# Kernel optimization log

Measured on AMD Instinct MI355X. Metric: run time of the kernel, lower is better.

Reference implementation:

```python
import jax, jax.numpy as jnp
import numpy as np

N_NODES = 100000
N_EDGES = 1600000
D_IN = 128
D_OUT = 128

def setup_inputs() -> dict:
    key = jax.random.key(0)
    k1, k2, k3, k4, k5 = jax.random.split(key, 5)
    h = jax.random.normal(k1, (N_NODES, D_IN), dtype=jnp.float32)
    src = jax.random.randint(k2, (N_EDGES,), 0, N_NODES, dtype=jnp.int64)
    dst = jax.random.randint(k3, (N_EDGES,), 0, N_NODES, dtype=jnp.int64)
    # Xavier-ish init for the two linear maps (fc_self, fc_neigh), no bias
    scale = 1.0 / np.sqrt(D_IN)
    W_self = jax.random.normal(k4, (D_IN, D_OUT), dtype=jnp.float32) * scale
    W_neigh = jax.random.normal(k5, (D_IN, D_OUT), dtype=jnp.float32) * scale
    return {"h": h, "src": src, "dst": dst, "W_self": W_self, "W_neigh": W_neigh}

def reference(h, src, dst, W_self, W_neigh):
    # DGL SAGEConv mean aggregator, bias=False:
    #   h_neigh[v] = mean_{(u->v) in E} h[u]   (0 if v has no in-edges)
    #   out = h @ W_self + h_neigh @ W_neigh
    msg = h[src]  # [E, D_IN] neighbor gather
    neigh_sum = jax.ops.segment_sum(msg, dst, num_segments=N_NODES)  # [N, D_IN]
    deg = jax.ops.segment_sum(jnp.ones((src.shape[0],), dtype=h.dtype), dst,
                              num_segments=N_NODES)  # [N]
    h_neigh = neigh_sum / jnp.maximum(deg, 1.0)[:, None]
    return h @ W_self + h_neigh @ W_neigh
```

## Files before the change

### kernel.cpp

```cpp
#include <hip/hip_runtime.h>


constexpr int NN = 100000;
constexpr int NE = 1600000;
constexpr int D  = 128;
constexpr int BK = 64;
constexpr int NB = (NN + BK - 1) / BK;
constexpr int PB = 8192;
constexpr int CAPB = 2048;
constexpr int XSTN = 136;
constexpr int PADI = 32;
constexpr int CVT_BLOCKS = NN * D / 8 / 256;

typedef __attribute__((ext_vector_type(8))) short short8;
typedef __attribute__((ext_vector_type(4))) float floatx4;
typedef __attribute__((ext_vector_type(2))) float floatx2;

static __device__ __forceinline__ unsigned short f2bf(float f) {
    unsigned u = __float_as_uint(f);
    unsigned r = ((u >> 16) & 1u) + 0x7fffu;
    return (unsigned short)((u + r) >> 16);
}

__global__ __launch_bounds__(256) void k_cvt(
    const float* __restrict__ h, const float* __restrict__ Wself,
    const float* __restrict__ Wneigh, uint2* __restrict__ hf8,
    unsigned short* __restrict__ Wp)
{
    const int t = threadIdx.x;
    if (blockIdx.x < CVT_BLOCKS) {
        int i = blockIdx.x * 256 + t;
        const float4* h4 = (const float4*)h;
        float4 a = h4[(size_t)i * 2];
        float4 b = h4[(size_t)i * 2 + 1];
        unsigned q0 = __builtin_amdgcn_cvt_pk_fp8_f32(a.x, a.y, 0u, false);
        q0          = __builtin_amdgcn_cvt_pk_fp8_f32(a.z, a.w, q0, true);
        unsigned q1 = __builtin_amdgcn_cvt_pk_fp8_f32(b.x, b.y, 0u, false);
        q1          = __builtin_amdgcn_cvt_pk_fp8_f32(b.z, b.w, q1, true);
        hf8[i] = make_uint2(q0, q1);
    } else {
        int kg  = (blockIdx.x - CVT_BLOCKS) * 2 + (t >> 7);
        int col = t & 127;
        unsigned short v[8];
#pragma unroll
        for (int j = 0; j < 8; ++j) {
            int k = kg * 8 + j;
            const float* W = (k < 128) ? (Wself + (size_t)k * D)
                                       : (Wneigh + (size_t)(k - 128) * D);
            v[j] = f2bf(W[col]);
        }
        uint4 o;
        o.x = (unsigned)v[0] | ((unsigned)v[1] << 16);
        o.y = (unsigned)v[2] | ((unsigned)v[3] << 16);
        o.z = (unsigned)v[4] | ((unsigned)v[5] << 16);
        o.w = (unsigned)v[6] | ((unsigned)v[7] << 16);
        ((uint4*)Wp)[kg * 128 + col] = o;
    }
}

__global__ __launch_bounds__(256) void k_part(
    const int* __restrict__ src, const int* __restrict__ dst,
    int* __restrict__ bcursor, unsigned* __restrict__ packed)
{
    __shared__ int lh[NB];
    const int t = threadIdx.x;
    const int e0 = blockIdx.x * PB;

    for (int i = t; i < NB; i += 256) lh[i] = 0;
    __syncthreads();

    int myd[32], msrc[32];
#pragma unroll
    for (int j = 0; j < 32; ++j) {
        int e = e0 + j * 256 + t;
        myd[j] = (e < NE) ? dst[e] : -1;
    }
#pragma unroll
    for (int j = 0; j < 32; ++j) {
        int e = e0 + j * 256 + t;
        msrc[j] = (e < NE) ? src[e] : 0;
    }
#pragma unroll
    for (int j = 0; j < 32; ++j)
        if (myd[j] >= 0) atomicAdd(&lh[myd[j] >> 6], 1);
    __syncthreads();
    for (int i = t; i < NB; i += 256) {
        int c = lh[i];
        if (c) lh[i] = atomicAdd(&bcursor[(size_t)i * PADI], c);
    }
    __syncthreads();
#pragma unroll
    for (int j = 0; j < 32; ++j) {
        if (myd[j] >= 0) {
            int b = myd[j] >> 6;
            int pos = atomicAdd(&lh[b], 1);
            packed[(size_t)b * CAPB + pos] =
                (unsigned)msrc[j] | ((unsigned)(myd[j] & 63) << 17);
        }
    }
}

__global__ __launch_bounds__(512, 8) void k_agg_gemm(
    const float* __restrict__ h, const uint2* __restrict__ hf8,
    const int* __restrict__ bcursor, const unsigned* __restrict__ packed,
    const unsigned short* __restrict__ Wp, float* __restrict__ out)
{
    __shared__ unsigned short Xs[BK][XSTN];
    __shared__ unsigned sorted[CAPB];
    __shared__ int cnt[BK], offs[BK], cur[BK];

    const int t      = threadIdx.x;
    const int bucket = blockIdx.x;
    const size_t ebeg = (size_t)bucket * CAPB;
    const int ecnt   = min(bcursor[(size_t)bucket * PADI], CAPB);

    if (t < BK) cnt[t] = 0;
    __syncthreads();

    unsigned pk[4];
#pragma unroll
    for (int i = 0; i < 4; ++i) {
        int idx = t + i * 512;
        pk[i] = (idx < ecnt) ? packed[ebeg + idx] : 0u;
    }
#pragma unroll
    for (int i = 0; i < 4; ++i) {
        int idx = t + i * 512;
        if (idx < ecnt) atomicAdd(&cnt[(pk[i] >> 17) & 63u], 1);
    }
    __syncthreads();
    if (t < BK) {
        int v = cnt[t];
        int sum = v;
#pragma unroll
        for (int off = 1; off < 64; off <<= 1) {
            int u = __shfl_up(sum, off, 64);
            if (t >= off) sum += u;
        }
        offs[t] = sum - v;
        cur[t]  = sum - v;
    }
    __syncthreads();
#pragma unroll
    for (int i = 0; i < 4; ++i) {
        int idx = t + i * 512;
        if (idx < ecnt) {
            int pos = atomicAdd(&cur[(pk[i] >> 17) & 63u], 1);
            sorted[pos] = pk[i] & 0x1FFFFu;
        }
    }
    __syncthreads();

    const int slot = t >> 4;
    const int l16  = t & 15;
#pragma unroll
    for (int ni = 0; ni < 2; ++ni) {
        int node = slot + ni * 32;
        const int beg = offs[node];
        const int n   = cnt[node];
        float a0[8] = {0,0,0,0,0,0,0,0};
        float a1[8] = {0,0,0,0,0,0,0,0};
        float a2[8] = {0,0,0,0,0,0,0,0};
        float a3[8] = {0,0,0,0,0,0,0,0};
        int e = 0;
        for (; e + 7 < n; e += 8) {
            uint2 x0 = hf8[(size_t)sorted[beg + e]     * 16 + l16];
            uint2 x1 = hf8[(size_t)sorted[beg + e + 1] * 16 + l16];
            uint2 x2 = hf8[(size_t)sorted[beg + e + 2] * 16 + l16];
            uint2 x3 = hf8[(size_t)sorted[beg + e + 3] * 16 + l16];
            uint2 x4 = hf8[(size_t)sorted[beg + e + 4] * 16 + l16];
            uint2 x5 = hf8[(size_t)sorted[beg + e + 5] * 16 + l16];
            uint2 x6 = hf8[(size_t)sorted[beg + e + 6] * 16 + l16];
            uint2 x7 = hf8[(size_t)sorted[beg + e + 7] * 16 + l16];
#pragma unroll
            for (int half = 0; half < 2; ++half) {
                unsigned w0 = half ? x0.y : x0.x, w1 = half ? x1.y : x1.x;
                unsigned w2 = half ? x2.y : x2.x, w3 = half ? x3.y : x3.x;
                unsigned w4 = half ? x4.y : x4.x, w5 = half ? x5.y : x5.x;
                unsigned w6 = half ? x6.y : x6.x, w7 = half ? x7.y : x7.x;
                floatx2 p;
                p = __builtin_amdgcn_cvt_pk_f32_fp8(w0, false); a0[half*4+0]+=p.x; a0[half*4+1]+=p.y;
                p = __builtin_amdgcn_cvt_pk_f32_fp8(w0, true);  a0[half*4+2]+=p.x; a0[half*4+3]+=p.y;
                p = __builtin_amdgcn_cvt_pk_f32_fp8(w1, false); a1[half*4+0]+=p.x; a1[half*4+1]+=p.y;
                p = __builtin_amdgcn_cvt_pk_f32_fp8(w1, true);  a1[half*4+2]+=p.x; a1[half*4+3]+=p.y;
                p = __builtin_amdgcn_cvt_pk_f32_fp8(w2, false); a2[half*4+0]+=p.x; a2[half*4+1]+=p.y;
                p = __builtin_amdgcn_cvt_pk_f32_fp8(w2, true);  a2[half*4+2]+=p.x; a2[half*4+3]+=p.y;
                p = __builtin_amdgcn_cvt_pk_f32_fp8(w3, false); a3[half*4+0]+=p.x; a3[half*4+1]+=p.y;
                p = __builtin_amdgcn_cvt_pk_f32_fp8(w3, true);  a3[half*4+2]+=p.x; a3[half*4+3]+=p.y;
                p = __builtin_amdgcn_cvt_pk_f32_fp8(w4, false); a0[half*4+0]+=p.x; a0[half*4+1]+=p.y;
                p = __builtin_amdgcn_cvt_pk_f32_fp8(w4, true);  a0[half*4+2]+=p.x; a0[half*4+3]+=p.y;
                p = __builtin_amdgcn_cvt_pk_f32_fp8(w5, false); a1[half*4+0]+=p.x; a1[half*4+1]+=p.y;
                p = __builtin_amdgcn_cvt_pk_f32_fp8(w5, true);  a1[half*4+2]+=p.x; a1[half*4+3]+=p.y;
                p = __builtin_amdgcn_cvt_pk_f32_fp8(w6, false); a2[half*4+0]+=p.x; a2[half*4+1]+=p.y;
                p = __builtin_amdgcn_cvt_pk_f32_fp8(w6, true);  a2[half*4+2]+=p.x; a2[half*4+3]+=p.y;
                p = __builtin_amdgcn_cvt_pk_f32_fp8(w7, false); a3[half*4+0]+=p.x; a3[half*4+1]+=p.y;
                p = __builtin_amdgcn_cvt_pk_f32_fp8(w7, true);  a3[half*4+2]+=p.x; a3[half*4+3]+=p.y;
            }
        }
        for (; e + 3 < n; e += 4) {
            uint2 x0 = hf8[(size_t)sorted[beg + e]     * 16 + l16];
            uint2 x1 = hf8[(size_t)sorted[beg + e + 1] * 16 + l16];
            uint2 x2 = hf8[(size_t)sorted[beg + e + 2] * 16 + l16];
            uint2 x3 = hf8[(size_t)sorted[beg + e + 3] * 16 + l16];
#pragma unroll
            for (int half = 0; half < 2; ++half) {
                unsigned w0 = half ? x0.y : x0.x, w1 = half ? x1.y : x1.x;
                unsigned w2 = half ? x2.y : x2.x, w3 = half ? x3.y : x3.x;
                floatx2 p;
                p = __builtin_amdgcn_cvt_pk_f32_fp8(w0, false); a0[half*4+0]+=p.x; a0[half*4+1]+=p.y;
                p = __builtin_amdgcn_cvt_pk_f32_fp8(w0, true);  a0[half*4+2]+=p.x; a0[half*4+3]+=p.y;
                p = __builtin_amdgcn_cvt_pk_f32_fp8(w1, false); a1[half*4+0]+=p.x; a1[half*4+1]+=p.y;
                p = __builtin_amdgcn_cvt_pk_f32_fp8(w1, true);  a1[half*4+2]+=p.x; a1[half*4+3]+=p.y;
                p = __builtin_amdgcn_cvt_pk_f32_fp8(w2, false); a2[half*4+0]+=p.x; a2[half*4+1]+=p.y;
                p = __builtin_amdgcn_cvt_pk_f32_fp8(w2, true);  a2[half*4+2]+=p.x; a2[half*4+3]+=p.y;
                p = __builtin_amdgcn_cvt_pk_f32_fp8(w3, false); a3[half*4+0]+=p.x; a3[half*4+1]+=p.y;
                p = __builtin_amdgcn_cvt_pk_f32_fp8(w3, true);  a3[half*4+2]+=p.x; a3[half*4+3]+=p.y;
            }
        }
        for (; e < n; ++e) {
            uint2 x = hf8[(size_t)sorted[beg + e] * 16 + l16];
#pragma unroll
            for (int half = 0; half < 2; ++half) {
                unsigned w = half ? x.y : x.x;
                floatx2 p;
                p = __builtin_amdgcn_cvt_pk_f32_fp8(w, false); a0[half*4+0]+=p.x; a0[half*4+1]+=p.y;
                p = __builtin_amdgcn_cvt_pk_f32_fp8(w, true);  a0[half*4+2]+=p.x; a0[half*4+3]+=p.y;
            }
        }
        float inv = (n > 0) ? 1.0f / (float)n : 0.0f;
        unsigned short m[8];
#pragma unroll
        for (int j = 0; j < 8; ++j)
            m[j] = f2bf((a0[j] + a1[j] + a2[j] + a3[j]) * inv);
        uint4 o;
        o.x = (unsigned)m[0] | ((unsigned)m[1] << 16);
        o.y = (unsigned)m[2] | ((unsigned)m[3] << 16);
        o.z = (unsigned)m[4] | ((unsigned)m[5] << 16);
        o.w = (unsigned)m[6] | ((unsigned)m[7] << 16);
        *(uint4*)&Xs[node][l16 * 8] = o;
    }
    __syncthreads();

    const int wave  = t >> 6;
    const int lane  = t & 63;
    const int wl16  = lane & 15;
    const int kg4   = lane >> 4;
    const int wrow  = wave & 3;
    const int chalf = wave >> 2;
    floatx4 acc[4];
#pragma unroll
    for (int c = 0; c < 4; ++c) acc[c] = (floatx4){0.f, 0.f, 0.f, 0.f};

    const int arow = wrow * 16 + wl16;
    const int grow = min(bucket * BK + arow, NN - 1);
    const float* hrow = h + (size_t)grow * D + kg4 * 8;

#pragma unroll
    for (int ks = 0; ks < 4; ++ks) {
        float4 f0 = *(const float4*)(hrow + ks * 32);
        float4 f1 = *(const float4*)(hrow + ks * 32 + 4);
        uint4 q;
        q.x = (unsigned)f2bf(f0.x) | ((unsigned)f2bf(f0.y) << 16);
        q.y = (unsigned)f2bf(f0.z) | ((unsigned)f2bf(f0.w) << 16);
        q.z = (unsigned)f2bf(f1.x) | ((unsigned)f2bf(f1.y) << 16);
        q.w = (unsigned)f2bf(f1.z) | ((unsigned)f2bf(f1.w) << 16);
        const short8 a = *(const short8*)&q;
#pragma unroll
        for (int c = 0; c < 4; ++c) {
            const int ct = chalf * 4 + c;
            const short8 b = *(const short8*)(Wp + (((ks * 4 + kg4) * 128) + ct * 16 + wl16) * 8);
            acc[c] = __builtin_amdgcn_mfma_f32_16x16x32_bf16(a, b, acc[c], 0, 0, 0);
        }
    }
#pragma unroll
    for (int ks = 4; ks < 8; ++ks) {
        const short8 a = *(const short8*)&Xs[arow][(ks - 4) * 32 + kg4 * 8];
#pragma unroll
        for (int c = 0; c < 4; ++c) {
            const int ct = chalf * 4 + c;
            const short8 b = *(const short8*)(Wp + (((ks * 4 + kg4) * 128) + ct * 16 + wl16) * 8);
            acc[c] = __builtin_amdgcn_mfma_f32_16x16x32_bf16(a, b, acc[c], 0, 0, 0);
        }
    }

    const int rbase = bucket * BK + wrow * 16 + kg4 * 4;
#pragma unroll
    for (int r = 0; r < 4; ++r) {
        int row = rbase + r;
        if (row < NN) {
            float* o = out + (size_t)row * D + chalf * 64 + wl16;
#pragma unroll
            for (int c = 0; c < 4; ++c)
                o[c * 16] = acc[c][r];
        }
    }
}

extern "C" void kernel_launch(void* const* d_in, const int* in_sizes, int n_in,
                              void* d_out, int out_size, void* d_ws, size_t ws_size,
                              hipStream_t stream) {
    const float* h      = (const float*)d_in[0];
    const int*   src    = (const int*)d_in[1];
    const int*   dst    = (const int*)d_in[2];
    const float* Wself  = (const float*)d_in[3];
    const float* Wneigh = (const float*)d_in[4];
    float*       out    = (float*)d_out;

    uint2* hf8         = (uint2*)d_ws;
    unsigned short* Wp = (unsigned short*)(hf8 + (size_t)NN * D / 8);
    unsigned* packed   = (unsigned*)(Wp + 256 * D);
    uintptr_t bc_a     = ((uintptr_t)(packed + (size_t)NB * CAPB) + 255) & ~(uintptr_t)255;
    int* bcursor       = (int*)bc_a;

    hipMemsetAsync(bcursor, 0, (size_t)NB * PADI * sizeof(int), stream);

    k_cvt      <<<dim3(CVT_BLOCKS + 16), 256, 0, stream>>>(h, Wself, Wneigh, hf8, Wp);
    k_part     <<<dim3((NE + PB - 1) / PB), 256, 0, stream>>>(src, dst, bcursor, packed);
    k_agg_gemm <<<dim3(NB), 512, 0, stream>>>(h, hf8, bcursor, packed, Wp, out);
}
```

Baseline: 192.3 us.

## Merge partition and conversion kernels; stage self rows in LDS; shrink gather unroll

Puts the edge partitioning, the weight packing and the fp8 feature conversion into one prep kernel, which removes a launch and lets the three independent jobs share the device. The first blocks do partitioning so the atomic-heavy work starts early. The aggregation kernel now loads and converts its own h rows to bf16 into a wider LDS tile up front, so the GEMM reads both halves of K from shared memory. The gather loop drops from 8-way to 4-way unrolling with two accumulator sets, and the occupancy hint drops from 8 to 6. This trades register pressure and memory-level parallelism for more LDS per block.

After: 183.4 us. 4.6% less time.

```diff
diff --git a/kernel.cpp b/kernel.cpp
--- a/kernel.cpp
+++ b/kernel.cpp
@@ -8,9 +8,11 @@
 constexpr int NB = (NN + BK - 1) / BK;
 constexpr int PB = 8192;
 constexpr int CAPB = 2048;
-constexpr int XSTN = 136;
+constexpr int XST = 264;
 constexpr int PADI = 32;
-constexpr int CVT_BLOCKS = NN * D / 8 / 256;
+constexpr int PART_BLOCKS = (NE + PB - 1) / PB;
+constexpr int WPK_BLOCKS  = 16;
+constexpr int CVT_BLOCKS  = NN * D / 8 / 256;
 
 typedef __attribute__((ext_vector_type(8))) short short8;
 typedef __attribute__((ext_vector_type(4))) float floatx4;
@@ -22,14 +24,68 @@
     return (unsigned short)((u + r) >> 16);
 }
 
-__global__ __launch_bounds__(256) void k_cvt(
+__global__ __launch_bounds__(256) void k_prep(
     const float* __restrict__ h, const float* __restrict__ Wself,
-    const float* __restrict__ Wneigh, uint2* __restrict__ hf8,
-    unsigned short* __restrict__ Wp)
+    const float* __restrict__ Wneigh, const int* __restrict__ src,
+    const int* __restrict__ dst, uint2* __restrict__ hf8,
+    unsigned short* __restrict__ Wp, int* __restrict__ bcursor,
+    unsigned* __restrict__ packed)
 {
     const int t = threadIdx.x;
-    if (blockIdx.x < CVT_BLOCKS) {
-        int i = blockIdx.x * 256 + t;
+    if (blockIdx.x < PART_BLOCKS) {
+        __shared__ int lh[NB];
+        const int e0 = blockIdx.x * PB;
+        for (int i = t; i < NB; i += 256) lh[i] = 0;
+        __syncthreads();
+
+        int myd[32], msrc[32];
+#pragma unroll
+        for (int j = 0; j < 32; ++j) {
+            int e = e0 + j * 256 + t;
+            myd[j] = (e < NE) ? dst[e] : -1;
+        }
+#pragma unroll
+        for (int j = 0; j < 32; ++j) {
+            int e = e0 + j * 256 + t;
+            msrc[j] = (e < NE) ? src[e] : 0;
+        }
+#pragma unroll
+        for (int j = 0; j < 32; ++j)
+            if (myd[j] >= 0) atomicAdd(&lh[myd[j] >> 6], 1);
+        __syncthreads();
+        for (int i = t; i < NB; i += 256) {
+            int c = lh[i];
+            if (c) lh[i] = atomicAdd(&bcursor[(size_t)i * PADI], c);
+        }
+        __syncthreads();
+#pragma unroll
+        for (int j = 0; j < 32; ++j) {
+            if (myd[j] >= 0) {
+                int b = myd[j] >> 6;
+                int pos = atomicAdd(&lh[b], 1);
+                packed[(size_t)b * CAPB + pos] =
+                    (unsigned)msrc[j] | ((unsigned)(myd[j] & 63) << 17);
+            }
+        }
+    } else if (blockIdx.x < PART_BLOCKS + WPK_BLOCKS) {
+        int kg  = (blockIdx.x - PART_BLOCKS) * 2 + (t >> 7);
+        int col = t & 127;
+        unsigned short v[8];
+#pragma unroll
+        for (int j = 0; j < 8; ++j) {
+            int k = kg * 8 + j;
+            const float* W = (k < 128) ? (Wself + (size_t)k * D)
+                                       : (Wneigh + (size_t)(k - 128) * D);
+            v[j] = f2bf(W[col]);
+        }
+        uint4 o;
+        o.x = (unsigned)v[0] | ((unsigned)v[1] << 16);
+        o.y = (unsigned)v[2] | ((unsigned)v[3] << 16);
+        o.z = (unsigned)v[4] | ((unsigned)v[5] << 16);
+        o.w = (unsigned)v[6] | ((unsigned)v[7] << 16);
+        ((uint4*)Wp)[kg * 128 + col] = o;
+    } else {
+        int i = (blockIdx.x - PART_BLOCKS - WPK_BLOCKS) * 256 + t;
         const float4* h4 = (const float4*)h;
         float4 a = h4[(size_t)i * 2];
         float4 b = h4[(size_t)i * 2 + 1];
@@ -38,74 +94,15 @@
         unsigned q1 = __builtin_amdgcn_cvt_pk_fp8_f32(b.x, b.y, 0u, false);
         q1          = __builtin_amdgcn_cvt_pk_fp8_f32(b.z, b.w, q1, true);
         hf8[i] = make_uint2(q0, q1);
-    } else {
-        int kg  = (blockIdx.x - CVT_BLOCKS) * 2 + (t >> 7);
-        int col = t & 127;
-        unsigned short v[8];
-#pragma unroll
-        for (int j = 0; j < 8; ++j) {
-            int k = kg * 8 + j;
-            const float* W = (k < 128) ? (Wself + (size_t)k * D)
-                                       : (Wneigh + (size_t)(k - 128) * D);
-            v[j] = f2bf(W[col]);
-        }
-        uint4 o;
-        o.x = (unsigned)v[0] | ((unsigned)v[1] << 16);
-        o.y = (unsigned)v[2] | ((unsigned)v[3] << 16);
-        o.z = (unsigned)v[4] | ((unsigned)v[5] << 16);
-        o.w = (unsigned)v[6] | ((unsigned)v[7] << 16);
-        ((uint4*)Wp)[kg * 128 + col] = o;
-    }
-}
-
-__global__ __launch_bounds__(256) void k_part(
-    const int* __restrict__ src, const int* __restrict__ dst,
-    int* __restrict__ bcursor, unsigned* __restrict__ packed)
-{
-    __shared__ int lh[NB];
-    const int t = threadIdx.x;
-    const int e0 = blockIdx.x * PB;
-
-    for (int i = t; i < NB; i += 256) lh[i] = 0;
-    __syncthreads();
-
-    int myd[32], msrc[32];
-#pragma unroll
-    for (int j = 0; j < 32; ++j) {
-        int e = e0 + j * 256 + t;
-        myd[j] = (e < NE) ? dst[e] : -1;
-    }
-#pragma unroll
-    for (int j = 0; j < 32; ++j) {
-        int e = e0 + j * 256 + t;
-        msrc[j] = (e < NE) ? src[e] : 0;
-    }
-#pragma unroll
-    for (int j = 0; j < 32; ++j)
-        if (myd[j] >= 0) atomicAdd(&lh[myd[j] >> 6], 1);
-    __syncthreads();
-    for (int i = t; i < NB; i += 256) {
-        int c = lh[i];
-        if (c) lh[i] = atomicAdd(&bcursor[(size_t)i * PADI], c);
-    }
-    __syncthreads();
-#pragma unroll
-    for (int j = 0; j < 32; ++j) {
-        if (myd[j] >= 0) {
-            int b = myd[j] >> 6;
-            int pos = atomicAdd(&lh[b], 1);
-            packed[(size_t)b * CAPB + pos] =
-                (unsigned)msrc[j] | ((unsigned)(myd[j] & 63) << 17);
-        }
-    }
-}
-
-__global__ __launch_bounds__(512, 8) void k_agg_gemm(
+    }
+}
+
+__global__ __launch_bounds__(512, 6) void k_agg_gemm(
     const float* __restrict__ h, const uint2* __restrict__ hf8,
     const int* __restrict__ bcursor, const unsigned* __restrict__ packed,
     const unsigned short* __restrict__ Wp, float* __restrict__ out)
 {
-    __shared__ unsigned short Xs[BK][XSTN];
+    __shared__ unsigned short Xs[BK][XST];
     __shared__ unsigned sorted[CAPB];
     __shared__ int cnt[BK], offs[BK], cur[BK];
 
@@ -115,6 +112,24 @@
     const int ecnt   = min(bcursor[(size_t)bucket * PADI], CAPB);
 
     if (t < BK) cnt[t] = 0;
+
+    {
+        int row = t >> 3, seg = t & 7;
+        int grow = min(bucket * BK + row, NN - 1);
+        const float4* hp = (const float4*)(h + (size_t)grow * D + seg * 16);
+        float4 f0 = hp[0], f1 = hp[1], f2 = hp[2], f3 = hp[3];
+        uint4 q0, q1;
+        q0.x = (unsigned)f2bf(f0.x) | ((unsigned)f2bf(f0.y) << 16);
+        q0.y = (unsigned)f2bf(f0.z) | ((unsigned)f2bf(f0.w) << 16);
+        q0.z = (unsigned)f2bf(f1.x) | ((unsigned)f2bf(f1.y) << 16);
+        q0.w = (unsigned)f2bf(f1.z) | ((unsigned)f2bf(f1.w) << 16);
+        q1.x = (unsigned)f2bf(f2.x) | ((unsigned)f2bf(f2.y) << 16);
+        q1.y = (unsigned)f2bf(f2.z) | ((unsigned)f2bf(f2.w) << 16);
+        q1.z = (unsigned)f2bf(f3.x) | ((unsigned)f2bf(f3.y) << 16);
+        q1.w = (unsigned)f2bf(f3.z) | ((unsigned)f2bf(f3.w) << 16);
+        *(uint4*)&Xs[row][seg * 16]     = q0;
+        *(uint4*)&Xs[row][seg * 16 + 8] = q1;
+    }
     __syncthreads();
 
     unsigned pk[4];
@@ -160,43 +175,7 @@
         const int n   = cnt[node];
         float a0[8] = {0,0,0,0,0,0,0,0};
         float a1[8] = {0,0,0,0,0,0,0,0};
-        float a2[8] = {0,0,0,0,0,0,0,0};
-        float a3[8] = {0,0,0,0,0,0,0,0};
         int e = 0;
-        for (; e + 7 < n; e += 8) {
-            uint2 x0 = hf8[(size_t)sorted[beg + e]     * 16 + l16];
-            uint2 x1 = hf8[(size_t)sorted[beg + e + 1] * 16 + l16];
-            uint2 x2 = hf8[(size_t)sorted[beg + e + 2] * 16 + l16];
-            uint2 x3 = hf8[(size_t)sorted[beg + e + 3] * 16 + l16];
-            uint2 x4 = hf8[(size_t)sorted[beg + e + 4] * 16 + l16];
-            uint2 x5 = hf8[(size_t)sorted[beg + e + 5] * 16 + l16];
-            uint2 x6 = hf8[(size_t)sorted[beg + e + 6] * 16 + l16];
-            uint2 x7 = hf8[(size_t)sorted[beg + e + 7] * 16 + l16];
-#pragma unroll
-            for (int half = 0; half < 2; ++half) {
-                unsigned w0 = half ? x0.y : x0.x, w1 = half ? x1.y : x1.x;
-                unsigned w2 = half ? x2.y : x2.x, w3 = half ? x3.y : x3.x;
-                unsigned w4 = half ? x4.y : x4.x, w5 = half ? x5.y : x5.x;
-                unsigned w6 = half ? x6.y : x6.x, w7 = half ? x7.y : x7.x;
-                floatx2 p;
-                p = __builtin_amdgcn_cvt_pk_f32_fp8(w0, false); a0[half*4+0]+=p.x; a0[half*4+1]+=p.y;
-                p = __builtin_amdgcn_cvt_pk_f32_fp8(w0, true);  a0[half*4+2]+=p.x; a0[half*4+3]+=p.y;
-                p = __builtin_amdgcn_cvt_pk_f32_fp8(w1, false); a1[half*4+0]+=p.x; a1[half*4+1]+=p.y;
-                p = __builtin_amdgcn_cvt_pk_f32_fp8(w1, true);  a1[half*4+2]+=p.x; a1[half*4+3]+=p.y;
-                p = __builtin_amdgcn_cvt_pk_f32_fp8(w2, false); a2[half*4+0]+=p.x; a2[half*4+1]+=p.y;
-                p = __builtin_amdgcn_cvt_pk_f32_fp8(w2, true);  a2[half*4+2]+=p.x; a2[half*4+3]+=p.y;
-                p = __builtin_amdgcn_cvt_pk_f32_fp8(w3, false); a3[half*4+0]+=p.x; a3[half*4+1]+=p.y;
-                p = __builtin_amdgcn_cvt_pk_f32_fp8(w3, true);  a3[half*4+2]+=p.x; a3[half*4+3]+=p.y;
-                p = __builtin_amdgcn_cvt_pk_f32_fp8(w4, false); a0[half*4+0]+=p.x; a0[half*4+1]+=p.y;
-                p = __builtin_amdgcn_cvt_pk_f32_fp8(w4, true);  a0[half*4+2]+=p.x; a0[half*4+3]+=p.y;
-                p = __builtin_amdgcn_cvt_pk_f32_fp8(w5, false); a1[half*4+0]+=p.x; a1[half*4+1]+=p.y;
-                p = __builtin_amdgcn_cvt_pk_f32_fp8(w5, true);  a1[half*4+2]+=p.x; a1[half*4+3]+=p.y;
-                p = __builtin_amdgcn_cvt_pk_f32_fp8(w6, false); a2[half*4+0]+=p.x; a2[half*4+1]+=p.y;
-                p = __builtin_amdgcn_cvt_pk_f32_fp8(w6, true);  a2[half*4+2]+=p.x; a2[half*4+3]+=p.y;
-                p = __builtin_amdgcn_cvt_pk_f32_fp8(w7, false); a3[half*4+0]+=p.x; a3[half*4+1]+=p.y;
-                p = __builtin_amdgcn_cvt_pk_f32_fp8(w7, true);  a3[half*4+2]+=p.x; a3[half*4+3]+=p.y;
-            }
-        }
         for (; e + 3 < n; e += 4) {
             uint2 x0 = hf8[(size_t)sorted[beg + e]     * 16 + l16];
             uint2 x1 = hf8[(size_t)sorted[beg + e + 1] * 16 + l16];
@@ -211,10 +190,10 @@
                 p = __builtin_amdgcn_cvt_pk_f32_fp8(w0, true);  a0[half*4+2]+=p.x; a0[half*4+3]+=p.y;
                 p = __builtin_amdgcn_cvt_pk_f32_fp8(w1, false); a1[half*4+0]+=p.x; a1[half*4+1]+=p.y;
                 p = __builtin_amdgcn_cvt_pk_f32_fp8(w1, true);  a1[half*4+2]+=p.x; a1[half*4+3]+=p.y;
-                p = __builtin_amdgcn_cvt_pk_f32_fp8(w2, false); a2[half*4+0]+=p.x; a2[half*4+1]+=p.y;
-                p = __builtin_amdgcn_cvt_pk_f32_fp8(w2, true);  a2[half*4+2]+=p.x; a2[half*4+3]+=p.y;
-                p = __builtin_amdgcn_cvt_pk_f32_fp8(w3, false); a3[half*4+0]+=p.x; a3[half*4+1]+=p.y;
-                p = __builtin_amdgcn_cvt_pk_f32_fp8(w3, true);  a3[half*4+2]+=p.x; a3[half*4+3]+=p.y;
+                p = __builtin_amdgcn_cvt_pk_f32_fp8(w2, false); a0[half*4+0]+=p.x; a0[half*4+1]+=p.y;
+                p = __builtin_amdgcn_cvt_pk_f32_fp8(w2, true);  a0[half*4+2]+=p.x; a0[half*4+3]+=p.y;
+                p = __builtin_amdgcn_cvt_pk_f32_fp8(w3, false); a1[half*4+0]+=p.x; a1[half*4+1]+=p.y;
+                p = __builtin_amdgcn_cvt_pk_f32_fp8(w3, true);  a1[half*4+2]+=p.x; a1[half*4+3]+=p.y;
             }
         }
         for (; e < n; ++e) {
@@ -231,13 +210,13 @@
         unsigned short m[8];
 #pragma unroll
         for (int j = 0; j < 8; ++j)
-            m[j] = f2bf((a0[j] + a1[j] + a2[j] + a3[j]) * inv);
+            m[j] = f2bf((a0[j] + a1[j]) * inv);
         uint4 o;
         o.x = (unsigned)m[0] | ((unsigned)m[1] << 16);
         o.y = (unsigned)m[2] | ((unsigned)m[3] << 16);
         o.z = (unsigned)m[4] | ((unsigned)m[5] << 16);
         o.w = (unsigned)m[6] | ((unsigned)m[7] << 16);
-        *(uint4*)&Xs[node][l16 * 8] = o;
+        *(uint4*)&Xs[node][128 + l16 * 8] = o;
     }
     __syncthreads();
 
@@ -252,29 +231,9 @@
     for (int c = 0; c < 4; ++c) acc[c] = (floatx4){0.f, 0.f, 0.f, 0.f};
 
     const int arow = wrow * 16 + wl16;
-    const int grow = min(bucket * BK + arow, NN - 1);
-    const float* hrow = h + (size_t)grow * D + kg4 * 8;
-
-#pragma unroll
-    for (int ks = 0; ks < 4; ++ks) {
-        float4 f0 = *(const float4*)(hrow + ks * 32);
-        float4 f1 = *(const float4*)(hrow + ks * 32 + 4);
-        uint4 q;
-        q.x = (unsigned)f2bf(f0.x) | ((unsigned)f2bf(f0.y) << 16);
-        q.y = (unsigned)f2bf(f0.z) | ((unsigned)f2bf(f0.w) << 16);
-        q.z = (unsigned)f2bf(f1.x) | ((unsigned)f2bf(f1.y) << 16);
-        q.w = (unsigned)f2bf(f1.z) | ((unsigned)f2bf(f1.w) << 16);
-        const short8 a = *(const short8*)&q;
-#pragma unroll
-        for (int c = 0; c < 4; ++c) {
-            const int ct = chalf * 4 + c;
-            const short8 b = *(const short8*)(Wp + (((ks * 4 + kg4) * 128) + ct * 16 + wl16) * 8);
-            acc[c] = __builtin_amdgcn_mfma_f32_16x16x32_bf16(a, b, acc[c], 0, 0, 0);
-        }
-    }
-#pragma unroll
-    for (int ks = 4; ks < 8; ++ks) {
-        const short8 a = *(const short8*)&Xs[arow][(ks - 4) * 32 + kg4 * 8];
+#pragma unroll
+    for (int ks = 0; ks < 8; ++ks) {
+        const short8 a = *(const short8*)&Xs[arow][ks * 32 + kg4 * 8];
 #pragma unroll
         for (int c = 0; c < 4; ++c) {
             const int ct = chalf * 4 + c;
@@ -314,7 +273,7 @@
 
     hipMemsetAsync(bcursor, 0, (size_t)NB * PADI * sizeof(int), stream);
 
-    k_cvt      <<<dim3(CVT_BLOCKS + 16), 256, 0, stream>>>(h, Wself, Wneigh, hf8, Wp);
-    k_part     <<<dim3((NE + PB - 1) / PB), 256, 0, stream>>>(src, dst, bcursor, packed);
+    k_prep     <<<dim3(PART_BLOCKS + WPK_BLOCKS + CVT_BLOCKS), 256, 0, stream>>>(
+                   h, Wself, Wneigh, src, dst, hf8, Wp, bcursor, packed);
     k_agg_gemm <<<dim3(NB), 512, 0, stream>>>(h, hf8, bcursor, packed, Wp, out);
 }
```
